# Optimization experiments

Measured on AMD Instinct MI355X. Metric: run time of the kernel, lower is better.

The kernel has to match this reference:

```python
import jax, jax.numpy as jnp
from jax import lax
import numpy as np

B, S, W = 32, 256, 16
WORD_VOCAB, WORD_DIM = 100000, 300
CHAR_VOCAB, CHAR_DIM = 101, 16  # len(char_vocab)+1
CH, WH = 16, 32                 # char_lstm_dim, lstm_size
GEN = 100
N_LABELS = 2


def _lstm(x, Wih, Whh, b, reverse=False):
    """Single-direction LSTM. x: [T, N, D]. Returns (outputs [T,N,H], final h [N,H]).
    Torch gate order: i, f, g, o."""
    pre = jnp.einsum('tnd,hd->tnh', x, Wih) + b  # [T, N, 4H]
    if reverse:
        pre = pre[::-1]
    H = Whh.shape[1]
    N = x.shape[1]

    def step(carry, xt):
        h, c = carry
        g = xt + h @ Whh.T
        i, f, gg, o = jnp.split(g, 4, axis=-1)
        c = jax.nn.sigmoid(f) * c + jax.nn.sigmoid(i) * jnp.tanh(gg)
        h = jax.nn.sigmoid(o) * jnp.tanh(c)
        return (h, c), h

    init = (jnp.zeros((N, H), x.dtype), jnp.zeros((N, H), x.dtype))
    (hT, _), hs = lax.scan(step, init, pre)
    if reverse:
        hs = hs[::-1]
    return hs, hT


def setup_inputs() -> dict:
    key = jax.random.key(0)
    ks = jax.random.split(key, 16)
    sc = lambda *shape: 0.1

    def rn(k, shape):
        return jax.random.normal(k, shape, dtype=jnp.float32) * 0.1

    return {
        'word_ids': jax.random.randint(ks[0], (B, S), 0, WORD_VOCAB),
        'char_ids': jax.random.randint(ks[1], (B, S, W), 0, CHAR_VOCAB),
        'word_table': rn(ks[2], (WORD_VOCAB, WORD_DIM)),
        'char_table': rn(ks[3], (CHAR_VOCAB, CHAR_DIM)),
        'c_Wih_f': rn(ks[4], (4 * CH, CHAR_DIM)), 'c_Whh_f': rn(ks[5], (4 * CH, CH)),
        'c_b_f': jnp.zeros((4 * CH,), jnp.float32),
        'c_Wih_b': rn(ks[6], (4 * CH, CHAR_DIM)), 'c_Whh_b': rn(ks[7], (4 * CH, CH)),
        'c_b_b': jnp.zeros((4 * CH,), jnp.float32),
        'gen_W': rn(ks[8], (GEN, WORD_DIM + 2 * CH)), 'gen_b': jnp.zeros((GEN,), jnp.float32),
        'w_Wih_f': rn(ks[9], (4 * WH, GEN)), 'w_Whh_f': rn(ks[10], (4 * WH, WH)),
        'w_b_f': jnp.zeros((4 * WH,), jnp.float32),
        'w_Wih_b': rn(ks[11], (4 * WH, GEN)), 'w_Whh_b': rn(ks[12], (4 * WH, WH)),
        'w_b_b': jnp.zeros((4 * WH,), jnp.float32),
        'out_W': rn(ks[13], (N_LABELS, 2 * WH)), 'out_b': jnp.zeros((N_LABELS,), jnp.float32),
    }


def reference(word_ids, char_ids, word_table, char_table,
              c_Wih_f, c_Whh_f, c_b_f, c_Wih_b, c_Whh_b, c_b_b,
              gen_W, gen_b,
              w_Wih_f, w_Whh_f, w_b_f, w_Wih_b, w_Whh_b, w_b_b,
              out_W, out_b):
    # Word embedding lookup: [B, S, WORD_DIM]
    word_e = word_table[word_ids]
    # Char embedding: [B, S, W, CHAR_DIM] -> char biLSTM over W, final states.
    char_e = char_table[char_ids].reshape(B * S, W, CHAR_DIM).transpose(1, 0, 2)  # [W, B*S, C]
    _, hf = _lstm(char_e, c_Wih_f, c_Whh_f, c_b_f, reverse=False)
    _, hb = _lstm(char_e, c_Wih_b, c_Whh_b, c_b_b, reverse=True)
    char_repr = jnp.concatenate([hf, hb], axis=-1).reshape(B, S, 2 * CH)
    # Concat word + char reprs, gen layer + gelu (dropout p=0 / eval).
    word_output = jnp.concatenate([word_e, char_repr], axis=-1)  # [B, S, 332]
    word_vecs = jax.nn.gelu(word_output @ gen_W.T + gen_b, approximate=False)  # [B, S, GEN]
    # Word-level biLSTM over S, per-step outputs.
    x = word_vecs.transpose(1, 0, 2)  # [S, B, GEN]
    of, _ = _lstm(x, w_Wih_f, w_Whh_f, w_b_f, reverse=False)
    ob, _ = _lstm(x, w_Wih_b, w_Whh_b, w_b_b, reverse=True)
    lstm_out = jnp.concatenate([of, ob], axis=-1).transpose(1, 0, 2)  # [B, S, 2*WH]
    # Output layer + sigmoid.
    return jax.nn.sigmoid(lstm_out @ out_W.T + out_b)  # [B, S, N_LABELS]
```

## Files before the change

kernel.cpp:

```cpp
#include <hip/hip_runtime.h>
#include <hip/hip_bf16.h>

#define B_    32
#define S_    256
#define BS_   8192
#define Wc_   16
#define CDIM_ 16
#define CH_   16
#define WDIM_ 300
#define KX_   332
#define XC_   336
#define GEN_  100
#define WVP_  104
#define WH_   32
#define NG_   128

constexpr size_t OFF_WV   = 0;
constexpr size_t OFF_PRE  = OFF_WV   + (size_t)BS_*WVP_;
constexpr size_t OFF_LO   = OFF_PRE  + (size_t)2*S_*B_*NG_;
constexpr size_t OFF_CHB  = OFF_LO   + (size_t)BS_*64;
constexpr size_t OFF_GWT  = OFF_CHB  + (size_t)BS_*32;
constexpr size_t OFF_WIHT = OFF_GWT  + (size_t)KX_*128;
constexpr size_t OFF_WHHT = OFF_WIHT + (size_t)2*GEN_*NG_;
constexpr size_t OFF_OW   = OFF_WHHT + (size_t)2*WH_*NG_;

__device__ __forceinline__ float sigm(float x){ return __builtin_amdgcn_rcpf(1.f + __expf(-x)); }
__device__ __forceinline__ float tanh_(float x){ return 1.f - 2.f*__builtin_amdgcn_rcpf(1.f + __expf(2.f*x)); }
__device__ __forceinline__ float rdlane(float v, int lane){
  return __uint_as_float(__builtin_amdgcn_readlane(__float_as_uint(v), lane));
}

__global__ void k_prep(const float* gen_W, const float* wih_f, const float* wih_b,
                       const float* whh_f, const float* whh_b, const float* out_W,
                       float* ws){
  int idx = blockIdx.x*blockDim.x + threadIdx.x;
  int stride = gridDim.x*blockDim.x;
  for (int i = idx; i < GEN_*KX_; i += stride){
    int j = i / KX_, k = i - j*KX_;
    ws[OFF_GWT + (size_t)k*128 + j] = gen_W[i];
  }
  for (int i = idx; i < NG_*GEN_; i += stride){
    int g = i / GEN_, k = i - g*GEN_;
    ws[OFF_WIHT + 0*GEN_*NG_ + (size_t)k*NG_ + g] = wih_f[i];
    ws[OFF_WIHT + 1*GEN_*NG_ + (size_t)k*NG_ + g] = wih_b[i];
  }
  for (int i = idx; i < NG_*WH_; i += stride){
    int g = i / WH_, k = i - g*WH_;
    ws[OFF_WHHT + 0*WH_*NG_ + (size_t)k*NG_ + g] = whh_f[i];
    ws[OFF_WHHT + 1*WH_*NG_ + (size_t)k*NG_ + g] = whh_b[i];
  }
  for (int i = idx; i < 2*64; i += stride) ws[OFF_OW + i] = out_W[i];
}

__global__ void __launch_bounds__(256, 2) k_char(const int* char_ids, const float* char_table,
                       const float* Wih_f, const float* Whh_f, const float* b_f,
                       const float* Wih_b, const float* Whh_b, const float* b_b,
                       float* ws){
  __shared__ float xr[16*324];
  const int dir = blockIdx.x & 1;
  const int sg  = blockIdx.x >> 1;
  const int tid = threadIdx.x;
  const float* WI = dir ? Wih_b : Wih_f;
  const float* WH = dir ? Whh_b : Whh_f;
  const float* BB = dir ? b_b  : b_f;
  const int ls = tid >> 4, u = tid & 15;
  const int seq0 = sg * 16;
  {
    const int id = char_ids[(seq0 + ls)*Wc_ + u];
    const float4* sr = (const float4*)(char_table + (size_t)id*CDIM_);
    float4 v0 = sr[0], v1 = sr[1], v2 = sr[2], v3 = sr[3];
    float* xw = &xr[ls*324 + u*20];
    *(float4*)(xw+0)  = v0; *(float4*)(xw+4)  = v1;
    *(float4*)(xw+8)  = v2; *(float4*)(xw+12) = v3;
  }
  float wi[4][16];
  #pragma unroll
  for (int g = 0; g < 4; ++g){
    const float4* wr = (const float4*)(WI + (size_t)(g*16+u)*CDIM_);
    float4 a = wr[0], b = wr[1], c = wr[2], d = wr[3];
    wi[g][0]=a.x; wi[g][1]=a.y; wi[g][2]=a.z; wi[g][3]=a.w;
    wi[g][4]=b.x; wi[g][5]=b.y; wi[g][6]=b.z; wi[g][7]=b.w;
    wi[g][8]=c.x; wi[g][9]=c.y; wi[g][10]=c.z; wi[g][11]=c.w;
    wi[g][12]=d.x; wi[g][13]=d.y; wi[g][14]=d.z; wi[g][15]=d.w;
  }
  float bias[4];
  #pragma unroll
  for (int g = 0; g < 4; ++g) bias[g] = BB[g*16+u];
  __syncthreads();
  float xp[16][4];
  const float* xb = &xr[ls*324];
  #pragma unroll
  for (int p = 0; p < 16; ++p){
    const int tm = dir ? (15-p) : p;
    const float4 x0 = *(const float4*)(xb + tm*20 + 0);
    const float4 x1 = *(const float4*)(xb + tm*20 + 4);
    const float4 x2 = *(const float4*)(xb + tm*20 + 8);
    const float4 x3 = *(const float4*)(xb + tm*20 + 12);
    float xk[16] = {x0.x,x0.y,x0.z,x0.w, x1.x,x1.y,x1.z,x1.w,
                    x2.x,x2.y,x2.z,x2.w, x3.x,x3.y,x3.z,x3.w};
    #pragma unroll
    for (int g = 0; g < 4; ++g){
      float a0 = bias[g], a1 = 0.f;
      #pragma unroll
      for (int k = 0; k < 16; k += 2){ a0 += wi[g][k]*xk[k]; a1 += wi[g][k+1]*xk[k+1]; }
      xp[p][g] = a0 + a1;
    }
  }
  float wh[4][16];
  #pragma unroll
  for (int g = 0; g < 4; ++g){
    const float4* wr = (const float4*)(WH + (size_t)(g*16+u)*CH_);
    float4 a = wr[0], b = wr[1], c = wr[2], d = wr[3];
    wh[g][0]=a.x; wh[g][1]=a.y; wh[g][2]=a.z; wh[g][3]=a.w;
    wh[g][4]=b.x; wh[g][5]=b.y; wh[g][6]=b.z; wh[g][7]=b.w;
    wh[g][8]=c.x; wh[g][9]=c.y; wh[g][10]=c.z; wh[g][11]=c.w;
    wh[g][12]=d.x; wh[g][13]=d.y; wh[g][14]=d.z; wh[g][15]=d.w;
  }
  const int lbase = (tid & 63) & 48;
  float h = 0.f, c = 0.f;
  #pragma unroll
  for (int p = 0; p < 16; ++p){
    float ai = xp[p][0], af = xp[p][1], ag = xp[p][2], ao = xp[p][3];
    #pragma unroll
    for (int k = 0; k < 16; ++k){
      const float hk = __shfl(h, lbase + k, 64);
      ai += wh[0][k]*hk; af += wh[1][k]*hk;
      ag += wh[2][k]*hk; ao += wh[3][k]*hk;
    }
    c = sigm(af)*c + sigm(ai)*tanh_(ag);
    h = sigm(ao)*tanh_(c);
  }
  ws[OFF_CHB + (size_t)(seq0 + ls)*32 + dir*16 + u] = h;
}

__global__ void k_gen(const int* word_ids, const float* word_table, const float* gen_b, float* ws){
  __shared__ __align__(16) float xt[16*XC_];
  __shared__ int wids[16];
  const int r0 = blockIdx.x*16;
  if (threadIdx.x < 16) wids[threadIdx.x] = word_ids[r0 + threadIdx.x];
  __syncthreads();
  float4* xt4 = (float4*)xt;
  for (int i = threadIdx.x; i < 16*75; i += 128){
    const int r = i/75, q = i - r*75;
    xt4[r*84 + q] = ((const float4*)(word_table + (size_t)wids[r]*WDIM_))[q];
  }
  for (int i = threadIdx.x; i < 16*8; i += 128){
    const int r = i >> 3, q = i & 7;
    xt4[r*84 + 75 + q] = ((const float4*)(ws + OFF_CHB + (size_t)(r0+r)*32))[q];
  }
  __syncthreads();
  const int j = threadIdx.x;
  const float bj = (j < GEN_) ? gen_b[j] : 0.f;
  float acc[16];
  #pragma unroll
  for (int r = 0; r < 16; ++r) acc[r] = bj;
  const float* WT = ws + OFF_GWT;
  for (int k4 = 0; k4 < KX_/4; ++k4){
    const int k = k4*4;
    const float w0 = WT[(size_t)(k+0)*128 + j];
    const float w1 = WT[(size_t)(k+1)*128 + j];
    const float w2 = WT[(size_t)(k+2)*128 + j];
    const float w3 = WT[(size_t)(k+3)*128 + j];
    #pragma unroll
    for (int r = 0; r < 16; ++r){
      const float4 xv = xt4[r*84 + k4];
      acc[r] += w0*xv.x + w1*xv.y + w2*xv.z + w3*xv.w;
    }
  }
  if (j < GEN_){
    float* wv = ws + OFF_WV;
    #pragma unroll
    for (int r = 0; r < 16; ++r){
      const float a = acc[r];
      wv[(size_t)(r0+r)*WVP_ + j] = 0.5f*a*(1.f + erff(a*0.70710678118f));
    }
  }
}

__global__ void k_wpre(const float* wb_f, const float* wb_b, float* ws){
  __shared__ __align__(16) float xt[8*WVP_];
  const int d  = blockIdx.x & 1;
  const int r0 = (blockIdx.x >> 1)*8;
  const float4* WVr = (const float4*)(ws + OFF_WV + (size_t)r0*WVP_);
  float4* xt4 = (float4*)xt;
  for (int i = threadIdx.x; i < 8*(WVP_/4); i += 128) xt4[i] = WVr[i];
  __syncthreads();
  const int g = threadIdx.x;
  const float wb = (d ? wb_b : wb_f)[g];
  float acc[8];
  #pragma unroll
  for (int r = 0; r < 8; ++r) acc[r] = wb;
  const float* WT = ws + OFF_WIHT + (size_t)d*GEN_*NG_;
  for (int k4 = 0; k4 < GEN_/4; ++k4){
    const int k = k4*4;
    const float w0 = WT[(size_t)(k+0)*NG_ + g];
    const float w1 = WT[(size_t)(k+1)*NG_ + g];
    const float w2 = WT[(size_t)(k+2)*NG_ + g];
    const float w3 = WT[(size_t)(k+3)*NG_ + g];
    #pragma unroll
    for (int r = 0; r < 8; ++r){
      const float4 xv = xt4[r*(WVP_/4) + k4];
      acc[r] += w0*xv.x + w1*xv.y + w2*xv.z + w3*xv.w;
    }
  }
  float* pre = ws + OFF_PRE + (size_t)d*S_*B_*NG_;
  #pragma unroll
  for (int r = 0; r < 8; ++r){
    const int row = r0 + r, b = row >> 8, s = row & 255;
    pre[((size_t)s*B_ + b)*NG_ + g] = acc[r];
  }
}

__global__ void __launch_bounds__(64) k_wlstm(const float* __restrict__ WHT,
                                              const float* __restrict__ PRE,
                                              float* __restrict__ LO){
  const int d = blockIdx.x >> 5;
  const int n = blockIdx.x & 31;
  const int l = threadIdx.x;
  const float* WT = WHT + (size_t)d*WH_*NG_;
  float wA[32], wB[32];
  #pragma unroll
  for (int k = 0; k < 32; ++k){ wA[k] = WT[(size_t)k*NG_ + l]; wB[k] = WT[(size_t)k*NG_ + 64 + l]; }
  const float* pre = PRE + (size_t)d*S_*B_*NG_ + (size_t)n*NG_;
  const float* p0 = pre + (size_t)(d ? (S_-1) : 0)*B_*NG_;
  const ptrdiff_t stp = (d ? -1 : 1) * (ptrdiff_t)(B_*NG_);
  float* loP = LO + (size_t)n*S_*64 + d*32 + l;
  float cst = 0.f, h = 0.f;

  float a0A = p0[0*stp + l], a0B = p0[0*stp + 64 + l];
  float a1A = p0[1*stp + l], a1B = p0[1*stp + 64 + l];
  float a2A = p0[2*stp + l], a2B = p0[2*stp + 64 + l];
  float a3A = p0[3*stp + l], a3B = p0[3*stp + 64 + l];

#define WSTEP(pAv, pBv, sidx) { \
    float aA0 = (pAv), aA1 = 0.f, aA2 = 0.f, aA3 = 0.f; \
    float aB0 = (pBv), aB1 = 0.f, aB2 = 0.f, aB3 = 0.f; \
    _Pragma("unroll") \
    for (int k = 0; k < 32; k += 4){ \
      const float h0 = rdlane(h, k+0); \
      const float h1 = rdlane(h, k+1); \
      const float h2 = rdlane(h, k+2); \
      const float h3 = rdlane(h, k+3); \
      aA0 += wA[k+0]*h0; aB0 += wB[k+0]*h0; \
      aA1 += wA[k+1]*h1; aB1 += wB[k+1]*h1; \
      aA2 += wA[k+2]*h2; aB2 += wB[k+2]*h2; \
      aA3 += wA[k+3]*h3; aB3 += wB[k+3]*h3; \
    } \
    const float aA = (aA0+aA1)+(aA2+aA3);    \
    const float aB = (aB0+aB1)+(aB2+aB3);    \
    const float fga = __shfl_xor(aA, 32); \
    const float oga = __shfl_xor(aB, 32); \
    const float cc = sigm(fga)*cst + sigm(aA)*tanh_(aB); \
    cst = cc; \
    h = sigm(oga)*tanh_(cc); \
    if (l < 32) loP[(size_t)(d ? (S_-1-(sidx)) : (sidx))*64] = h; \
  }

  for (int t = 0; t < S_; t += 4){
    float n0A=0.f, n0B=0.f, n1A=0.f, n1B=0.f, n2A=0.f, n2B=0.f, n3A=0.f, n3B=0.f;
    if (t + 4 < S_){
      const float* q = p0 + (ptrdiff_t)(t+4)*stp;
      n0A = q[0*stp + l]; n0B = q[0*stp + 64 + l];
      n1A = q[1*stp + l]; n1B = q[1*stp + 64 + l];
      n2A = q[2*stp + l]; n2B = q[2*stp + 64 + l];
      n3A = q[3*stp + l]; n3B = q[3*stp + 64 + l];
    }
    WSTEP(a0A, a0B, t+0)
    WSTEP(a1A, a1B, t+1)
    WSTEP(a2A, a2B, t+2)
    WSTEP(a3A, a3B, t+3)
    a0A=n0A; a0B=n0B; a1A=n1A; a1B=n1B;
    a2A=n2A; a2B=n2B; a3A=n3A; a3B=n3B;
  }
#undef WSTEP
}

__global__ void k_out(const float* ws, const float* out_b, float* out){
  const int row = blockIdx.x*blockDim.x + threadIdx.x;
  const float4* lo = (const float4*)(ws + OFF_LO + (size_t)row*64);
  const float* OW = ws + OFF_OW;
  float a0 = out_b[0], a1 = out_b[1];
  #pragma unroll
  for (int q = 0; q < 16; ++q){
    const float4 v = lo[q];
    a0 += OW[q*4+0]*v.x + OW[q*4+1]*v.y + OW[q*4+2]*v.z + OW[q*4+3]*v.w;
    a1 += OW[64+q*4+0]*v.x + OW[64+q*4+1]*v.y + OW[64+q*4+2]*v.z + OW[64+q*4+3]*v.w;
  }
  out[row*2+0] = sigm(a0);
  out[row*2+1] = sigm(a1);
}

extern "C" void kernel_launch(void* const* d_in, const int* in_sizes, int n_in,
                              void* d_out, int out_size, void* d_ws, size_t ws_size,
                              hipStream_t stream){
  (void)in_sizes; (void)n_in; (void)out_size; (void)ws_size;
  const int*   word_ids   = (const int*)  d_in[0];
  const int*   char_ids   = (const int*)  d_in[1];
  const float* word_table = (const float*)d_in[2];
  const float* char_table = (const float*)d_in[3];
  const float* c_Wih_f    = (const float*)d_in[4];
  const float* c_Whh_f    = (const float*)d_in[5];
  const float* c_b_f      = (const float*)d_in[6];
  const float* c_Wih_b    = (const float*)d_in[7];
  const float* c_Whh_b    = (const float*)d_in[8];
  const float* c_b_b      = (const float*)d_in[9];
  const float* gen_W      = (const float*)d_in[10];
  const float* gen_b      = (const float*)d_in[11];
  const float* w_Wih_f    = (const float*)d_in[12];
  const float* w_Whh_f    = (const float*)d_in[13];
  const float* w_b_f      = (const float*)d_in[14];
  const float* w_Wih_b    = (const float*)d_in[15];
  const float* w_Whh_b    = (const float*)d_in[16];
  const float* w_b_b      = (const float*)d_in[17];
  const float* out_W      = (const float*)d_in[18];
  const float* out_b      = (const float*)d_in[19];
  float* ws  = (float*)d_ws;
  float* out = (float*)d_out;

  hipLaunchKernelGGL(k_prep,  dim3(64),   dim3(256), 0, stream,
                     gen_W, w_Wih_f, w_Wih_b, w_Whh_f, w_Whh_b, out_W, ws);
  hipLaunchKernelGGL(k_char,  dim3(1024), dim3(256), 0, stream,
                     char_ids, char_table, c_Wih_f, c_Whh_f, c_b_f,
                     c_Wih_b, c_Whh_b, c_b_b, ws);
  hipLaunchKernelGGL(k_gen,   dim3(512),  dim3(128), 0, stream, word_ids, word_table, gen_b, ws);
  hipLaunchKernelGGL(k_wpre,  dim3(2048), dim3(128), 0, stream, w_b_f, w_b_b, ws);
  hipLaunchKernelGGL(k_wlstm, dim3(64),   dim3(64),  0, stream,
                     ws + OFF_WHHT, ws + OFF_PRE, ws + OFF_LO);
  hipLaunchKernelGGL(k_out,   dim3(64),   dim3(128), 0, stream, ws, out_b, out);
}
```

Baseline: 191.9 us.

## Move word-LSTM recurrent weights to LDS and batch hidden-state stores

The recurrent weights for the word-level LSTM are moved from 64 per-thread registers into a padded shared-memory array and read back as float4 vectors each step. Per-step hidden-state outputs are buffered in LDS and written to global memory in coalesced float4 chunks every 32 steps, replacing scattered per-step scalar stores. This lowers register pressure and global store traffic, but adds LDS reads to the serial recurrence critical path. Cross-lane ordering on the LDS staging buffer relies on single-wavefront execution, since there is no barrier before the flush.

Result: slower. 236.1 us (+23.0%).

```diff
diff --git a/kernel.cpp b/kernel.cpp
--- a/kernel.cpp
+++ b/kernel.cpp
@@ -211,20 +211,27 @@
   }
 }
 
+#define HR_ (64*68)
 __global__ void __launch_bounds__(64) k_wlstm(const float* __restrict__ WHT,
                                               const float* __restrict__ PRE,
                                               float* __restrict__ LO){
-  const int d = blockIdx.x >> 5;
-  const int n = blockIdx.x & 31;
+  __shared__ __align__(16) float arr[64*68 + 32*36];
+  const int pair = blockIdx.x;
+  const int d = pair >> 5;
+  const int n = pair & 31;
   const int l = threadIdx.x;
   const float* WT = WHT + (size_t)d*WH_*NG_;
-  float wA[32], wB[32];
-  #pragma unroll
-  for (int k = 0; k < 32; ++k){ wA[k] = WT[(size_t)k*NG_ + l]; wB[k] = WT[(size_t)k*NG_ + 64 + l]; }
+  for (int i = l; i < 64*64; i += 64){
+    const int k = i >> 6, row = i & 63;
+    const float v = (k < 32) ? WT[(size_t)k*NG_ + row]
+                             : WT[(size_t)(k-32)*NG_ + 64 + row];
+    arr[row*68 + k] = v;
+  }
+  __syncthreads();
+
   const float* pre = PRE + (size_t)d*S_*B_*NG_ + (size_t)n*NG_;
   const float* p0 = pre + (size_t)(d ? (S_-1) : 0)*B_*NG_;
   const ptrdiff_t stp = (d ? -1 : 1) * (ptrdiff_t)(B_*NG_);
-  float* loP = LO + (size_t)n*S_*64 + d*32 + l;
   float cst = 0.f, h = 0.f;
 
   float a0A = p0[0*stp + l], a0B = p0[0*stp + 64 + l];
@@ -233,27 +240,28 @@
   float a3A = p0[3*stp + l], a3B = p0[3*stp + 64 + l];
 
 #define WSTEP(pAv, pBv, sidx) { \
-    float aA0 = (pAv), aA1 = 0.f, aA2 = 0.f, aA3 = 0.f; \
-    float aB0 = (pBv), aB1 = 0.f, aB2 = 0.f, aB3 = 0.f; \
+    float aA0 = (pAv), aA1 = 0.f; \
+    float aB0 = (pBv), aB1 = 0.f; \
+    const float* wl = &arr[l*68]; \
     _Pragma("unroll") \
-    for (int k = 0; k < 32; k += 4){ \
-      const float h0 = rdlane(h, k+0); \
-      const float h1 = rdlane(h, k+1); \
-      const float h2 = rdlane(h, k+2); \
-      const float h3 = rdlane(h, k+3); \
-      aA0 += wA[k+0]*h0; aB0 += wB[k+0]*h0; \
-      aA1 += wA[k+1]*h1; aB1 += wB[k+1]*h1; \
-      aA2 += wA[k+2]*h2; aB2 += wB[k+2]*h2; \
-      aA3 += wA[k+3]*h3; aB3 += wB[k+3]*h3; \
+    for (int kk = 0; kk < 32; kk += 4){ \
+      const float4 wa = *(const float4*)(wl + kk); \
+      const float4 wb = *(const float4*)(wl + 32 + kk); \
+      const float h0 = rdlane(h, kk+0); \
+      const float h1 = rdlane(h, kk+1); \
+      const float h2 = rdlane(h, kk+2); \
+      const float h3 = rdlane(h, kk+3); \
+      aA0 += wa.x*h0 + wa.y*h1; aA1 += wa.z*h2 + wa.w*h3; \
+      aB0 += wb.x*h0 + wb.y*h1; aB1 += wb.z*h2 + wb.w*h3; \
     } \
-    const float aA = (aA0+aA1)+(aA2+aA3);    \
-    const float aB = (aB0+aB1)+(aB2+aB3);    \
+    const float aA = aA0 + aA1;            \
+    const float aB = aB0 + aB1;            \
     const float fga = __shfl_xor(aA, 32); \
     const float oga = __shfl_xor(aB, 32); \
-    const float cc = sigm(fga)*cst + sigm(aA)*tanh_(aB); \
+    const float cc = sigm(fga)*cst + sigm(aA)*tanh_(aB);   \
     cst = cc; \
-    h = sigm(oga)*tanh_(cc); \
-    if (l < 32) loP[(size_t)(d ? (S_-1-(sidx)) : (sidx))*64] = h; \
+    h = sigm(oga)*tanh_(cc);                                \
+    if (l < 32) arr[HR_ + ((sidx) & 31)*36 + l] = h; \
   }
 
   for (int t = 0; t < S_; t += 4){
@@ -271,6 +279,16 @@
     WSTEP(a3A, a3B, t+3)
     a0A=n0A; a0B=n0B; a1A=n1A; a1B=n1B;
     a2A=n2A; a2B=n2B; a3A=n3A; a3B=n3B;
+
+    if ((t & 31) == 28){
+      const int s0 = t & ~31;
+      const int srow = l >> 1, half = l & 1;
+      const int s = s0 + srow;
+      const int ss = d ? (S_ - 1 - s) : s;
+      const float4* src = (const float4*)&arr[HR_ + srow*36 + half*16];
+      float4* dst = (float4*)(LO + ((size_t)n*S_ + ss)*64 + d*32 + half*16);
+      dst[0] = src[0]; dst[1] = src[1]; dst[2] = src[2]; dst[3] = src[3];
+    }
   }
 #undef WSTEP
 }
```
